# Kernel optimization log

Hardware: AMD Instinct MI355X
Metric: run time of the kernel (lower is better)

## Reference

```python
import jax, jax.numpy as jnp
import numpy as np

B, IN_FEATURES, UNITS, BITS = 64, 1024, 1024, 8


def setup_inputs() -> dict:
    key = jax.random.key(0)
    k1, k2, k3 = jax.random.split(key, 3)
    # Quantized integer activations stored as float32 (TF code does int math).
    x = jax.random.randint(k1, (B, IN_FEATURES), 0, 16).astype(jnp.float32)
    # Low-bit integer weights: BITS-bit signed magnitude, |w| < 4**(BITS//2).
    kernel = jax.random.randint(k2, (IN_FEATURES, UNITS), -128, 128).astype(jnp.float32)
    bias = jax.random.randint(k3, (UNITS,), -32, 32).astype(jnp.float32)
    return {"x": x, "kernel": kernel, "bias": bias, "bits": BITS}


def reference(x, kernel, bias, bits):
    # Faithful vectorized version of the TF bit-serial quantized matmul.
    # TF per-feature loop is vectorized over the input-feature axis; the
    # small fixed loop over 2-bit weight chunks is kept (bits//2 iterations).
    nchunks = bits // 2
    sgn = jnp.sign(kernel)            # (In, U)
    wa = jnp.abs(kernel)              # (In, U)
    x3 = x[:, :, None]                # (B, In, 1)
    d = jnp.zeros((x.shape[0], x.shape[1], kernel.shape[1]), x.dtype)  # (B, In, U)
    for _ in range(nchunks):
        c = (wa % 4.0) * sgn          # current 2-bit chunk, re-signed
        d = d + x3 * c[None, :, :]
        wa = jnp.trunc(wa / 4.0)      # tf.cast(w/4, int32): trunc toward 0 (w >= 0)
        d = jnp.trunc(d / 4.0)        # tf.cast(dim1/4, int32): trunc toward 0
    res = d.sum(axis=1)               # (B, U), accumulation over input features
    return jax.nn.relu(res + bias)    # activation == 'relu' branch
```

## Files before the change

### kernel.cpp

```cpp
#include <hip/hip_runtime.h>

#define IN_F   1024
#define UNITS  1024
#define BDIM   64
#define NCH    8
#define CHUNK  128
#define BG     4


__global__ __launch_bounds__(256) void partial_kernel(
    const float* __restrict__ x, const float* __restrict__ K,
    float* __restrict__ ws)
{
    const int bid = blockIdx.x;
    const int jt = bid & 3;
    const int bg = (bid >> 2) & 15;
    const int ic = bid >> 6;
    const int tid = threadIdx.x;
    const int j  = jt * 256 + tid;
    const int b0 = bg * BG;
    const int i0 = ic * CHUNK;

    __shared__ float xs[CHUNK * BG];
    for (int t = tid; t < CHUNK * BG; t += 256) {
        const int bb = t >> 7;
        const int ii = t & 127;
        xs[ii * BG + bb] = x[(b0 + bb) * IN_F + i0 + ii] * (1.0f / 256.0f);
    }
    __syncthreads();

    float acc0 = 0.f, acc1 = 0.f, acc2 = 0.f, acc3 = 0.f;
    const float* kp = K + (size_t)i0 * UNITS + j;
#pragma unroll 8
    for (int i = 0; i < CHUNK; ++i) {
        const float k = kp[(size_t)i * UNITS];
        const float4 xv = *(const float4*)&xs[i * BG];
        acc0 += truncf(xv.x * k);
        acc1 += truncf(xv.y * k);
        acc2 += truncf(xv.z * k);
        acc3 += truncf(xv.w * k);
    }

    float* wp = ws + ((size_t)ic * BDIM + b0) * UNITS + j;
    wp[0 * UNITS] = acc0;
    wp[1 * UNITS] = acc1;
    wp[2 * UNITS] = acc2;
    wp[3 * UNITS] = acc3;
}

__global__ __launch_bounds__(256) void reduce_kernel(
    const float* __restrict__ ws, const float* __restrict__ bias,
    float* __restrict__ out)
{
    const int idx = blockIdx.x * 256 + threadIdx.x;
    const int j4 = idx & 255;
    const int b  = idx >> 8;

    const float4* p = (const float4*)ws + (size_t)b * (UNITS / 4) + j4;
    float4 s = make_float4(0.f, 0.f, 0.f, 0.f);
#pragma unroll
    for (int c = 0; c < NCH; ++c) {
        const float4 v = p[(size_t)c * BDIM * (UNITS / 4)];
        s.x += v.x; s.y += v.y; s.z += v.z; s.w += v.w;
    }
    const float4 bv = ((const float4*)bias)[j4];
    s.x = fmaxf(s.x + bv.x, 0.f);
    s.y = fmaxf(s.y + bv.y, 0.f);
    s.z = fmaxf(s.z + bv.z, 0.f);
    s.w = fmaxf(s.w + bv.w, 0.f);
    ((float4*)out)[idx] = s;
}

extern "C" void kernel_launch(void* const* d_in, const int* in_sizes, int n_in,
                              void* d_out, int out_size, void* d_ws, size_t ws_size,
                              hipStream_t stream) {
    const float* x    = (const float*)d_in[0];
    const float* K    = (const float*)d_in[1];
    const float* bias = (const float*)d_in[2];
    float* out = (float*)d_out;
    float* ws  = (float*)d_ws;

    partial_kernel<<<512, 256, 0, stream>>>(x, K, ws);
    reduce_kernel<<<64, 256, 0, stream>>>(ws, bias, out);
}
```

Baseline: 73.37 us.

## Widen per-thread tile to 4 units with float4 loads, split input features finer

Each thread of the partial kernel now computes a 4x4 tile (4 batches × 4 units) from vectorized float4 loads of the weight row, so one block covers all 1024 units. The input-feature chunk shrinks from 128 to 32, giving 32 chunks × 16 batch groups = 512 blocks. The reduce kernel now sums 32 partials instead of 8 and runs as 128 blocks of 128 threads. The intent is fewer, wider loads and more ILP per thread, paid for with a 4x larger workspace to write and read in the reduction.

New measurement: 74.05 us. No clear change (+0.9%).

```diff
diff --git a/kernel.cpp b/kernel.cpp
--- a/kernel.cpp
+++ b/kernel.cpp
@@ -3,9 +3,10 @@
 #define IN_F   1024
 #define UNITS  1024
 #define BDIM   64
-#define NCH    8
-#define CHUNK  128
+#define NCH    32
+#define CHUNK  32
 #define BG     4
+#define NBG    16
 
 
 __global__ __launch_bounds__(256) void partial_kernel(
@@ -13,46 +14,50 @@
     float* __restrict__ ws)
 {
     const int bid = blockIdx.x;
-    const int jt = bid & 3;
-    const int bg = (bid >> 2) & 15;
-    const int ic = bid >> 6;
-    const int tid = threadIdx.x;
-    const int j  = jt * 256 + tid;
+    const int bg = bid & (NBG - 1);
+    const int ic = bid >> 4;
+    const int t  = threadIdx.x;
     const int b0 = bg * BG;
     const int i0 = ic * CHUNK;
 
     __shared__ float xs[CHUNK * BG];
-    for (int t = tid; t < CHUNK * BG; t += 256) {
-        const int bb = t >> 7;
-        const int ii = t & 127;
+    if (t < CHUNK * BG) {
+        const int ii = t >> 2;
+        const int bb = t & 3;
         xs[ii * BG + bb] = x[(b0 + bb) * IN_F + i0 + ii] * (1.0f / 256.0f);
     }
     __syncthreads();
 
-    float acc0 = 0.f, acc1 = 0.f, acc2 = 0.f, acc3 = 0.f;
-    const float* kp = K + (size_t)i0 * UNITS + j;
-#pragma unroll 8
+    float4 acc0 = make_float4(0.f, 0.f, 0.f, 0.f);
+    float4 acc1 = acc0, acc2 = acc0, acc3 = acc0;
+
+    const float4* kp = (const float4*)(K + (size_t)i0 * UNITS) + t;
+#pragma unroll 4
     for (int i = 0; i < CHUNK; ++i) {
-        const float k = kp[(size_t)i * UNITS];
+        const float4 k4 = kp[(size_t)i * (UNITS / 4)];
         const float4 xv = *(const float4*)&xs[i * BG];
-        acc0 += truncf(xv.x * k);
-        acc1 += truncf(xv.y * k);
-        acc2 += truncf(xv.z * k);
-        acc3 += truncf(xv.w * k);
+        acc0.x += truncf(xv.x * k4.x); acc0.y += truncf(xv.x * k4.y);
+        acc0.z += truncf(xv.x * k4.z); acc0.w += truncf(xv.x * k4.w);
+        acc1.x += truncf(xv.y * k4.x); acc1.y += truncf(xv.y * k4.y);
+        acc1.z += truncf(xv.y * k4.z); acc1.w += truncf(xv.y * k4.w);
+        acc2.x += truncf(xv.z * k4.x); acc2.y += truncf(xv.z * k4.y);
+        acc2.z += truncf(xv.z * k4.z); acc2.w += truncf(xv.z * k4.w);
+        acc3.x += truncf(xv.w * k4.x); acc3.y += truncf(xv.w * k4.y);
+        acc3.z += truncf(xv.w * k4.z); acc3.w += truncf(xv.w * k4.w);
     }
 
-    float* wp = ws + ((size_t)ic * BDIM + b0) * UNITS + j;
-    wp[0 * UNITS] = acc0;
-    wp[1 * UNITS] = acc1;
-    wp[2 * UNITS] = acc2;
-    wp[3 * UNITS] = acc3;
+    float4* wp = (float4*)(ws + ((size_t)ic * BDIM + b0) * UNITS) + t;
+    wp[0 * (UNITS / 4)] = acc0;
+    wp[1 * (UNITS / 4)] = acc1;
+    wp[2 * (UNITS / 4)] = acc2;
+    wp[3 * (UNITS / 4)] = acc3;
 }
 
-__global__ __launch_bounds__(256) void reduce_kernel(
+__global__ __launch_bounds__(128) void reduce_kernel(
     const float* __restrict__ ws, const float* __restrict__ bias,
     float* __restrict__ out)
 {
-    const int idx = blockIdx.x * 256 + threadIdx.x;
+    const int idx = blockIdx.x * 128 + threadIdx.x;
     const int j4 = idx & 255;
     const int b  = idx >> 8;
 
@@ -80,6 +85,6 @@
     float* out = (float*)d_out;
     float* ws  = (float*)d_ws;
 
-    partial_kernel<<<512, 256, 0, stream>>>(x, K, ws);
-    reduce_kernel<<<64, 256, 0, stream>>>(ws, bias, out);
+    partial_kernel<<<NBG * NCH, 256, 0, stream>>>(x, K, ws);
+    reduce_kernel<<<128, 128, 0, stream>>>(ws, bias, out);
 }
```
